# Kernel tuning notes

Hardware: AMD Instinct MI355X
Metric: run time of the kernel (lower is better)

## Reference

```python
import jax, jax.numpy as jnp
import numpy as np

TREE_DEPTH = 6
IN_F, OUT_F = 1024, 1024
BATCH = 2048
N_LEAVES = 2 ** TREE_DEPTH
N_NODES = N_LEAVES - 1


def _tree_routes(depth):
    """Static routing table: for each leaf, the decision-node index visited at
    each depth and whether the leaf takes the sigmoid (1) or 1-sigmoid (0) branch.
    Mirrors the torch traversal: node = 2*node + 1 + bit; bits of leaf id LSB-first."""
    n_leaves = 2 ** depth
    idx = np.zeros((n_leaves, depth), dtype=np.int32)
    pos = np.zeros((n_leaves, depth), dtype=bool)
    for l in range(n_leaves):
        node, index = 0, l
        for d in range(depth):
            idx[l, d] = node
            pos[l, d] = (index % 2 == 0)
            node = node * 2 + 1 + index % 2
            index >>= 1
    return idx, pos

ROUTE_IDX, ROUTE_POS = _tree_routes(TREE_DEPTH)


def setup_inputs() -> dict:
    key = jax.random.key(0)
    kx, kwd, kwl = jax.random.split(key, 3)
    scale = 0.02  # keep sigmoid/softmax logits in a sane range
    x = jax.random.normal(kx, (BATCH, IN_F), dtype=jnp.float32)
    Wd = jax.random.normal(kwd, (N_NODES, IN_F), dtype=jnp.float32) * scale
    bd = jnp.zeros((N_NODES,), dtype=jnp.float32)
    Wl = jax.random.normal(kwl, (N_LEAVES, OUT_F, IN_F), dtype=jnp.float32) * scale
    bl = jnp.zeros((N_LEAVES, OUT_F), dtype=jnp.float32)
    return {"x": x, "Wd": Wd, "bd": bd, "Wl": Wl, "bl": bl}


def reference(x, Wd, bd, Wl, bl):
    # All decision node probabilities in one GEMM: [B, n_nodes]
    dprob = jax.nn.sigmoid(x @ Wd.T + bd)
    # Gather per-leaf path probs [B, L, depth] and take path product -> routing [B, L]
    path = dprob[:, ROUTE_IDX]                      # [B, L, D]
    path = jnp.where(ROUTE_POS, path, 1.0 - path)
    routing = jnp.prod(path, axis=-1)               # [B, L]
    # All leaf experts in one batched GEMM: [B, L, out], softmax over out (torch dim=1)
    leaf_logits = jnp.einsum('bi,loi->blo', x, Wl) + bl
    leaves = jax.nn.softmax(leaf_logits, axis=-1)
    # Routing-weighted sum over leaves
    return jnp.einsum('bl,blo->bo', routing, leaves)
```

## Files before the change

### kernel.cpp

```cpp
#include <hip/hip_runtime.h>
#include <hip/hip_bf16.h>

#define BATCH 2048
#define KD 1024
#define ND 1024
#define NLEAF 64
#define BM 256
#define BN 256

typedef __attribute__((ext_vector_type(8))) short bf16x8;
typedef __attribute__((ext_vector_type(4))) float f32x4;
typedef __attribute__((ext_vector_type(4))) _Float16 f16x4;

#define WLB_OFF 0ULL
#define XP_OFF  134217728ULL
#define RT_OFF  138412032ULL
#define LG_OFF  138936320ULL

__device__ __forceinline__ unsigned short f2bf(float f) {
  unsigned int u = __float_as_uint(f);
  u += 0x7fffu + ((u >> 16) & 1u);
  return (unsigned short)(u >> 16);
}

__device__ __forceinline__ void gload_lds16(const void* g, void* l) {
  __builtin_amdgcn_global_load_lds(
      (const __attribute__((address_space(1))) unsigned int*)g,
      (__attribute__((address_space(3))) unsigned int*)l, 16, 0, 0);
}

__global__ void __launch_bounds__(256) convert_kernel(
    const float* __restrict__ Wl, const float* __restrict__ x,
    unsigned short* __restrict__ wlb, unsigned short* __restrict__ xp) {
  const long long WL4 = 16777216LL;
  const long long XJ  = 524288LL;
  long long i = (long long)blockIdx.x * 256 + threadIdx.x;
  const long long stride = (long long)gridDim.x * 256;
  for (; i < WL4 + XJ; i += stride) {
    if (i < WL4) {
      float4 v = ((const float4*)Wl)[i];
      ushort4 o;
      o.x = f2bf(v.x); o.y = f2bf(v.y); o.z = f2bf(v.z); o.w = f2bf(v.w);
      ((ushort4*)wlb)[i] = o;
    } else {
      const long long jj = i - WL4;
      const int pt = (int)(jj >> 1), half = (int)(jj & 1);
      const int f = pt >> 6, l = pt & 63;
      const int row = (f & 127) * 16 + (l & 15);
      const int k0 = (f >> 7) * 32 + (l >> 4) * 8 + half * 4;
      float4 v = *(const float4*)(x + (size_t)row * KD + k0);
      ushort4 o;
      o.x = f2bf(v.x); o.y = f2bf(v.y); o.z = f2bf(v.z); o.w = f2bf(v.w);
      *(ushort4*)(xp + (size_t)f * 512 + l * 8 + half * 4) = o;
    }
  }
}

__global__ void __launch_bounds__(256) routing_kernel(
    const float* __restrict__ x, const float* __restrict__ Wd,
    const float* __restrict__ bd, float* __restrict__ rt) {
  __shared__ float xs[4][KD];
  __shared__ float sdp[4][64];
  const int tid = threadIdx.x;
  const int b0 = blockIdx.x * 4;
  const float4* xsrc = (const float4*)(x + (size_t)b0 * KD);
  float4* xdst = (float4*)&xs[0][0];
  for (int i = tid; i < KD; i += 256) xdst[i] = xsrc[i];
  __syncthreads();
  const int wv = tid >> 6, ln = tid & 63;
  const int b = b0 + wv;
  if (ln < 63) {
    const float4* wrow = (const float4*)(Wd + (size_t)ln * KD);
    const float4* xr = (const float4*)&xs[wv][0];
    float4 a = {0.f, 0.f, 0.f, 0.f};
    for (int k = 0; k < KD / 4; ++k) {
      float4 w = wrow[k], xv = xr[k];
      a.x += w.x * xv.x; a.y += w.y * xv.y; a.z += w.z * xv.z; a.w += w.w * xv.w;
    }
    float z = a.x + a.y + a.z + a.w + bd[ln];
    sdp[wv][ln] = 1.f / (1.f + __expf(-z));
  }
  __syncthreads();
  float prod = 1.f;
  int node = 0, index = ln;
  for (int d = 0; d < 6; ++d) {
    float pv = sdp[wv][node];
    prod *= (index & 1) ? (1.f - pv) : pv;
    node = node * 2 + 1 + (index & 1);
    index >>= 1;
  }
  rt[(size_t)b * NLEAF + ln] = prod;
}

#define GBODY(CUR, NXT, S, VMASM, LAST)                                     \
  {                                                                          \
    if (!(LAST)) {                                                           \
      _Pragma("unroll")                                                      \
      for (int mi = 0; mi < 8; ++mi)                                         \
        NXT[mi] = *(const bf16x8*)(apL +                                     \
            ((size_t)((S) + 1) * 128 + rf0 + mi) * 512);                     \
    }                                                                        \
    if ((S) + 2 < 32) STAGE_B((S) + 2);                                      \
    asm volatile(VMASM ::: "memory");                                        \
    asm volatile("s_barrier" ::: "memory");                                  \
    const char* bbuf = smem + ((S) & 3) * 16384;                             \
    bf16x8 bfr[4];                                                           \
    _Pragma("unroll")                                                        \
    for (int ni = 0; ni < 4; ++ni)                                           \
      bfr[ni] = *(const bf16x8*)(bbuf + offB[ni]);                           \
    __builtin_amdgcn_s_setprio(1);                                           \
    _Pragma("unroll")                                                        \
    for (int mi = 0; mi < 8; ++mi)                                           \
      _Pragma("unroll")                                                      \
      for (int ni = 0; ni < 4; ++ni)                                         \
        acc[mi][ni] = __builtin_amdgcn_mfma_f32_16x16x32_bf16(               \
            CUR[mi], bfr[ni], acc[mi][ni], 0, 0, 0);                         \
    __builtin_amdgcn_s_setprio(0);                                           \
  }

__global__ void __launch_bounds__(512, 2) gemm_kernel(
    const unsigned short* __restrict__ Ap, const unsigned short* __restrict__ B,
    _Float16* __restrict__ C, int ntile) {
  extern __shared__ char smem[];
  const int tid = threadIdx.x;
  const int w = tid >> 6, ln = tid & 63;
  const int wm = w >> 2, wn = w & 3;
  const int g = ln >> 4, r16 = ln & 15;
  const int bid = blockIdx.x;
  const int j = bid >> 3;
  const int bm = (j & 7) * BM;
  const int bn = (((j >> 3) << 3) + (bid & 7)) * BN;
  const long long ldc = (long long)ntile * 256;

  const int rS = tid >> 2;
  const int cS = tid & 3;
  const int csrc = cS ^ ((rS >> 1) & 3);
  const unsigned short* gb0 = B + (size_t)(bn + rS) * KD + csrc * 8;
  const unsigned short* gb1 = gb0 + (size_t)128 * KD;
  const int ldsw = w * 1024;

  auto STAGE_B = [&](int s) {
    char* base = smem + (s & 3) * 16384;
    const size_t ko = (size_t)s * 32;
    gload_lds16(gb0 + ko, base + ldsw);
    gload_lds16(gb1 + ko, base + 8192 + ldsw);
  };

  int offB[4];
#pragma unroll
  for (int ni = 0; ni < 4; ++ni) {
    const int row = wn * 64 + ni * 16 + r16;
    offB[ni] = row * 64 + (g ^ ((row >> 1) & 3)) * 16;
  }

  const int rf0 = (bm >> 4) + wm * 8;
  const unsigned short* apL = Ap + (size_t)ln * 8;

  f32x4 acc[8][4];
#pragma unroll
  for (int mi = 0; mi < 8; ++mi)
#pragma unroll
    for (int ni = 0; ni < 4; ++ni) acc[mi][ni] = (f32x4){0.f, 0.f, 0.f, 0.f};

  bf16x8 aE[8], aO[8];
  STAGE_B(0);
#pragma unroll
  for (int mi = 0; mi < 8; ++mi)
    aE[mi] = *(const bf16x8*)(apL + ((size_t)rf0 + mi) * 512);
  STAGE_B(1);

  for (int u = 0; u < 15; ++u) {
    GBODY(aE, aO, 2 * u,     "s_waitcnt vmcnt(10)", false);
    GBODY(aO, aE, 2 * u + 1, "s_waitcnt vmcnt(10)", false);
  }
  GBODY(aE, aO, 30, "s_waitcnt vmcnt(8)", false);
  GBODY(aO, aE, 31, "s_waitcnt vmcnt(0)", true);

#pragma unroll
  for (int mi = 0; mi < 8; ++mi)
#pragma unroll
    for (int q = 0; q < 4; ++q) {
      const long long grow = bm + wm * 128 + mi * 16 + g * 4 + q;
#pragma unroll
      for (int ni = 0; ni < 4; ++ni) {
        const int gcol = bn + wn * 64 + ni * 16 + r16;
        C[grow * ldc + gcol] = (_Float16)acc[mi][ni][q];
      }
    }
}

__global__ void __launch_bounds__(256) smax_kernel(
    const _Float16* __restrict__ Cg, const float* __restrict__ rt,
    const float* __restrict__ bl, float* __restrict__ out,
    int lpg, int l0, int first) {
  __shared__ float reds[2][2][4];
  __shared__ float rts[64];
  const int tid = threadIdx.x;
  const int b = blockIdx.x;
  const int w = tid >> 6, ln = tid & 63;
  const int c0 = tid * 4;
  if (tid < lpg) rts[tid] = rt[(size_t)b * NLEAF + l0 + tid];
  __syncthreads();
  float oacc[4] = {0.f, 0.f, 0.f, 0.f};
  const long long ldc = (long long)lpg * ND;

  for (int jj = 0; jj < lpg; jj += 2) {
    const int par = (jj >> 1) & 1;
    const f16x4 h0 = *(const f16x4*)(Cg + (size_t)b * ldc + jj * ND + c0);
    const f16x4 h1 = *(const f16x4*)(Cg + (size_t)b * ldc + (jj + 1) * ND + c0);
    const float4 bv0 = *(const float4*)(bl + (size_t)(l0 + jj) * ND + c0);
    const float4 bv1 = *(const float4*)(bl + (size_t)(l0 + jj + 1) * ND + c0);
    float e0[4], e1[4], s0 = 0.f, s1 = 0.f;
    e0[0] = __expf((float)h0[0] + bv0.x); e0[1] = __expf((float)h0[1] + bv0.y);
    e0[2] = __expf((float)h0[2] + bv0.z); e0[3] = __expf((float)h0[3] + bv0.w);
    e1[0] = __expf((float)h1[0] + bv1.x); e1[1] = __expf((float)h1[1] + bv1.y);
    e1[2] = __expf((float)h1[2] + bv1.z); e1[3] = __expf((float)h1[3] + bv1.w);
#pragma unroll
    for (int k = 0; k < 4; ++k) { s0 += e0[k]; s1 += e1[k]; }
#pragma unroll
    for (int off = 1; off < 64; off <<= 1) {
      s0 += __shfl_xor(s0, off);
      s1 += __shfl_xor(s1, off);
    }
    if (ln == 0) { reds[par][0][w] = s0; reds[par][1][w] = s1; }
    __syncthreads();
    const float S0 = reds[par][0][0] + reds[par][0][1] + reds[par][0][2] + reds[par][0][3];
    const float S1 = reds[par][1][0] + reds[par][1][1] + reds[par][1][2] + reds[par][1][3];
    const float c0f = rts[jj] / S0;
    const float c1f = rts[jj + 1] / S1;
#pragma unroll
    for (int k = 0; k < 4; ++k) oacc[k] += c0f * e0[k] + c1f * e1[k];
  }

  float* orow = out + (size_t)b * ND + c0;
  if (first) {
    *(float4*)orow = (float4){oacc[0], oacc[1], oacc[2], oacc[3]};
  } else {
    float4 p = *(const float4*)orow;
    p.x += oacc[0]; p.y += oacc[1]; p.z += oacc[2]; p.w += oacc[3];
    *(float4*)orow = p;
  }
}

extern "C" void kernel_launch(void* const* d_in, const int* in_sizes, int n_in,
                              void* d_out, int out_size, void* d_ws, size_t ws_size,
                              hipStream_t stream) {
  const float* x  = (const float*)d_in[0];
  const float* Wd = (const float*)d_in[1];
  const float* bd = (const float*)d_in[2];
  const float* Wl = (const float*)d_in[3];
  const float* bl = (const float*)d_in[4];
  float* out = (float*)d_out;
  char* ws = (char*)d_ws;
  unsigned short* wlb = (unsigned short*)(ws + WLB_OFF);
  unsigned short* xp  = (unsigned short*)(ws + XP_OFF);
  float* rt           = (float*)(ws + RT_OFF);
  _Float16* lg        = (_Float16*)(ws + LG_OFF);

  convert_kernel<<<2048, 256, 0, stream>>>(Wl, x, wlb, xp);
  routing_kernel<<<BATCH / 4, 256, 0, stream>>>(x, Wd, bd, rt);
  hipFuncSetAttribute((const void*)gemm_kernel,
                      hipFuncAttributeMaxDynamicSharedMemorySize, 65536);

  const int ngrp = (ws_size >= LG_OFF + (size_t)BATCH * NLEAF * ND * 2) ? 1 : 4;
  const int lpg = NLEAF / ngrp;
  const int ntile = lpg * (ND / BN);
  for (int grp = 0; grp < ngrp; ++grp) {
    gemm_kernel<<<8 * ntile, 512, 65536, stream>>>(
        xp, wlb + (size_t)grp * lpg * ND * KD, lg, ntile);
    smax_kernel<<<BATCH, 256, 0, stream>>>(lg, rt, bl, out,
                                           lpg, grp * lpg, grp == 0);
  }
}
```

Measured before the change: 554.0 us.

## Give each wave a private B slice in LDS and drop block barriers

The GEMM tile shrinks from 256x256 with 8 waves to 128x256 with 4 waves. Each wave stages its own 64-column slice of B into a private LDS region, so the per-stage s_barrier goes away and only vmcnt/lgkmcnt waits remain. The B prefetch depth rises from 2 to 3 stages, and the block-to-tile mapping is rearranged so blocks are spread across XCDs. In exchange, every A fragment is now shared by fewer waves, which adds A traffic, and the grid doubles.

```diff
diff --git a/kernel.cpp b/kernel.cpp
--- a/kernel.cpp
+++ b/kernel.cpp
@@ -5,7 +5,7 @@
 #define KD 1024
 #define ND 1024
 #define NLEAF 64
-#define BM 256
+#define BM 128
 #define BN 256
 
 typedef __attribute__((ext_vector_type(8))) short bf16x8;
@@ -92,7 +92,7 @@
   rt[(size_t)b * NLEAF + ln] = prod;
 }
 
-#define GBODY(CUR, NXT, S, VMASM, LAST)                                     \
+#define GBODY(CUR, NXT, S, VMASM, LAST)                                      \
   {                                                                          \
     if (!(LAST)) {                                                           \
       _Pragma("unroll")                                                      \
@@ -100,14 +100,15 @@
         NXT[mi] = *(const bf16x8*)(apL +                                     \
             ((size_t)((S) + 1) * 128 + rf0 + mi) * 512);                     \
     }                                                                        \
-    if ((S) + 2 < 32) STAGE_B((S) + 2);                                      \
+    if ((S) + 3 < 32) STAGE_B((S) + 3);                                      \
     asm volatile(VMASM ::: "memory");                                        \
-    asm volatile("s_barrier" ::: "memory");                                  \
-    const char* bbuf = smem + ((S) & 3) * 16384;                             \
+    const char* bbuf = myB + (((S) & 3) * 4096);                             \
     bf16x8 bfr[4];                                                           \
     _Pragma("unroll")                                                        \
     for (int ni = 0; ni < 4; ++ni)                                           \
       bfr[ni] = *(const bf16x8*)(bbuf + offB[ni]);                           \
+    asm volatile("s_waitcnt lgkmcnt(0)" ::: "memory");                       \
+    __builtin_amdgcn_sched_barrier(0);                                       \
     __builtin_amdgcn_s_setprio(1);                                           \
     _Pragma("unroll")                                                        \
     for (int mi = 0; mi < 8; ++mi)                                           \
@@ -118,42 +119,43 @@
     __builtin_amdgcn_s_setprio(0);                                           \
   }
 
-__global__ void __launch_bounds__(512, 2) gemm_kernel(
+__global__ void __launch_bounds__(256, 2) gemm_kernel(
     const unsigned short* __restrict__ Ap, const unsigned short* __restrict__ B,
     _Float16* __restrict__ C, int ntile) {
   extern __shared__ char smem[];
   const int tid = threadIdx.x;
   const int w = tid >> 6, ln = tid & 63;
-  const int wm = w >> 2, wn = w & 3;
   const int g = ln >> 4, r16 = ln & 15;
   const int bid = blockIdx.x;
-  const int j = bid >> 3;
-  const int bm = (j & 7) * BM;
-  const int bn = (((j >> 3) << 3) + (bid & 7)) * BN;
+  const int cpx = gridDim.x >> 3;
+  const int wg = (bid & 7) * cpx + (bid >> 3);
+  const int mt = wg & 15, nt = wg >> 4;
+  const int bm = mt * BM;
+  const int bn = nt * BN;
   const long long ldc = (long long)ntile * 256;
 
-  const int rS = tid >> 2;
-  const int cS = tid & 3;
-  const int csrc = cS ^ ((rS >> 1) & 3);
-  const unsigned short* gb0 = B + (size_t)(bn + rS) * KD + csrc * 8;
-  const unsigned short* gb1 = gb0 + (size_t)128 * KD;
-  const int ldsw = w * 1024;
+  const int rB = ln >> 2;
+  const int csrcB = (ln & 3) ^ ((rB >> 1) & 3);
+  const unsigned short* gbw =
+      B + (size_t)(bn + w * 64 + rB) * KD + csrcB * 8;
+  char* myB = smem + w * 16384;
 
   auto STAGE_B = [&](int s) {
-    char* base = smem + (s & 3) * 16384;
+    char* base = myB + ((s & 3) * 4096);
     const size_t ko = (size_t)s * 32;
-    gload_lds16(gb0 + ko, base + ldsw);
-    gload_lds16(gb1 + ko, base + 8192 + ldsw);
+#pragma unroll
+    for (int it = 0; it < 4; ++it)
+      gload_lds16(gbw + (size_t)it * 16 * KD + ko, base + it * 1024);
   };
 
   int offB[4];
 #pragma unroll
   for (int ni = 0; ni < 4; ++ni) {
-    const int row = wn * 64 + ni * 16 + r16;
-    offB[ni] = row * 64 + (g ^ ((row >> 1) & 3)) * 16;
-  }
-
-  const int rf0 = (bm >> 4) + wm * 8;
+    const int lr = ni * 16 + r16;
+    offB[ni] = lr * 64 + (g ^ ((lr >> 1) & 3)) * 16;
+  }
+
+  const int rf0 = bm >> 4;
   const unsigned short* apL = Ap + (size_t)ln * 8;
 
   f32x4 acc[8][4];
@@ -168,22 +170,25 @@
   for (int mi = 0; mi < 8; ++mi)
     aE[mi] = *(const bf16x8*)(apL + ((size_t)rf0 + mi) * 512);
   STAGE_B(1);
-
-  for (int u = 0; u < 15; ++u) {
-    GBODY(aE, aO, 2 * u,     "s_waitcnt vmcnt(10)", false);
-    GBODY(aO, aE, 2 * u + 1, "s_waitcnt vmcnt(10)", false);
-  }
-  GBODY(aE, aO, 30, "s_waitcnt vmcnt(8)", false);
-  GBODY(aO, aE, 31, "s_waitcnt vmcnt(0)", true);
+  STAGE_B(2);
+
+  for (int u = 0; u < 14; ++u) {
+    GBODY(aE, aO, 2 * u,     "s_waitcnt vmcnt(20)", false);
+    GBODY(aO, aE, 2 * u + 1, "s_waitcnt vmcnt(20)", false);
+  }
+  GBODY(aE, aO, 28, "s_waitcnt vmcnt(20)", false);
+  GBODY(aO, aE, 29, "s_waitcnt vmcnt(16)", false);
+  GBODY(aE, aO, 30, "s_waitcnt vmcnt(12)", false);
+  GBODY(aO, aE, 31, "s_waitcnt vmcnt(0)",  true);
 
 #pragma unroll
   for (int mi = 0; mi < 8; ++mi)
 #pragma unroll
     for (int q = 0; q < 4; ++q) {
-      const long long grow = bm + wm * 128 + mi * 16 + g * 4 + q;
+      const long long grow = bm + mi * 16 + g * 4 + q;
 #pragma unroll
       for (int ni = 0; ni < 4; ++ni) {
-        const int gcol = bn + wn * 64 + ni * 16 + r16;
+        const int gcol = bn + w * 64 + ni * 16 + r16;
         C[grow * ldc + gcol] = (_Float16)acc[mi][ni][q];
       }
     }
@@ -266,7 +271,7 @@
   const int lpg = NLEAF / ngrp;
   const int ntile = lpg * (ND / BN);
   for (int grp = 0; grp < ngrp; ++grp) {
-    gemm_kernel<<<8 * ntile, 512, 65536, stream>>>(
+    gemm_kernel<<<16 * ntile, 256, 65536, stream>>>(
         xp, wlb + (size_t)grp * lpg * ND * KD, lg, ntile);
     smax_kernel<<<BATCH, 256, 0, stream>>>(lg, rt, bl, out,
                                            lpg, grp * lpg, grp == 0);
```

Result: faster. 534.3 us (-3.6%).
